# Optimization experiments

Measured on AMD Instinct MI355X. Metric: run time of the kernel, lower is better.

## Reference

```python
import jax, jax.numpy as jnp
import numpy as np

DIM = 768
NH = 12
HD = DIM // NH
MLP = 4 * DIM
EPS = 1e-5


def _ln(x, w, b):
    mu = x.mean(-1, keepdims=True)
    var = ((x - mu) ** 2).mean(-1, keepdims=True)
    return (x - mu) * jax.lax.rsqrt(var + EPS) * w + b


def setup_inputs() -> dict:
    key = jax.random.key(0)
    ks = jax.random.split(key, 12)
    s = 0.02
    return {
        "xq": jax.random.normal(ks[0], (4, 32, 32, DIM), jnp.float32),
        "xkv": jax.random.normal(ks[1], (4, 64, 64, DIM), jnp.float32),
        "norm1_w": jnp.ones((DIM,), jnp.float32),
        "norm1_b": jnp.zeros((DIM,), jnp.float32),
        "kv_w": jax.random.normal(ks[2], (DIM, 2 * DIM), jnp.float32) * s,
        "kv_b": jnp.zeros((2 * DIM,), jnp.float32),
        "q_w": jax.random.normal(ks[3], (DIM, DIM), jnp.float32) * s,
        "q_b": jnp.zeros((DIM,), jnp.float32),
        "proj_w": jax.random.normal(ks[4], (DIM, DIM), jnp.float32) * s,
        "proj_b": jnp.zeros((DIM,), jnp.float32),
        "norm2_w": jnp.ones((DIM,), jnp.float32),
        "norm2_b": jnp.zeros((DIM,), jnp.float32),
        "mlp_w1": jax.random.normal(ks[5], (DIM, MLP), jnp.float32) * s,
        "mlp_b1": jnp.zeros((MLP,), jnp.float32),
        "mlp_w2": jax.random.normal(ks[6], (MLP, DIM), jnp.float32) * s,
        "mlp_b2": jnp.zeros((DIM,), jnp.float32),
    }


def reference(xq, xkv, norm1_w, norm1_b, kv_w, kv_b, q_w, q_b, proj_w, proj_b,
              norm2_w, norm2_b, mlp_w1, mlp_b1, mlp_w2, mlp_b2):
    B, Hq, Wq, C = xq.shape
    _, H, W, _ = xkv.shape
    shortcut = xq
    xn = _ln(xq, norm1_w, norm1_b)
    # kv projection: [B, H*W, 2, NH, HD]
    kv = (xkv.reshape(B, H * W, C) @ kv_w + kv_b).reshape(B, H * W, 2, NH, HD)
    k = kv[:, :, 0].transpose(0, 2, 1, 3)  # [B, NH, HW, HD]
    v = kv[:, :, 1].transpose(0, 2, 1, 3)
    q = (xn.reshape(B, Hq * Wq, C) @ q_w + q_b).reshape(B, Hq * Wq, NH, HD).transpose(0, 2, 1, 3)
    scale = HD ** -0.5
    attn = jnp.einsum('bhqd,bhkd->bhqk', q * scale, k)
    attn = jax.nn.softmax(attn, axis=-1)
    o = jnp.einsum('bhqk,bhkd->bhqd', attn, v)  # [B, NH, HqWq, HD]
    o = o.transpose(0, 2, 1, 3).reshape(B, Hq, Wq, C)
    o = o @ proj_w + proj_b
    x = shortcut + o
    xn2 = _ln(x, norm2_w, norm2_b)
    mlp = jax.nn.gelu(xn2 @ mlp_w1 + mlp_b1, approximate=False) @ mlp_w2 + mlp_b2
    return x + mlp
```

## Files before the change

kernel.cpp:

```cpp
#include <hip/hip_runtime.h>
#include <hip/hip_bf16.h>
#include <math.h>

#define DIM 768
#define NH 12
#define HD 64
#define NQ 1024
#define NKV 4096
#define QSCALE 0.18033688011112042f

typedef __attribute__((ext_vector_type(4))) float f32x4;
typedef __attribute__((ext_vector_type(16))) float f32x16;
typedef __attribute__((ext_vector_type(8))) __bf16 bf16x8;
typedef __attribute__((ext_vector_type(8))) unsigned short u16x8;
typedef __attribute__((ext_vector_type(4))) unsigned short u16x4;
typedef unsigned short u16;

typedef const __attribute__((address_space(1))) void* gas_t;
typedef __attribute__((address_space(3))) void* las_t;

__device__ __forceinline__ void gl16(const void* g, void* l) {
    __builtin_amdgcn_global_load_lds((gas_t)g, (las_t)l, 16, 0, 0);
}

__device__ __forceinline__ u16 f2b(float x) {
    __bf16 h = (__bf16)x;
    return __builtin_bit_cast(u16, h);
}

__device__ __forceinline__ float b2f(u16 x) {
    unsigned int u = ((unsigned int)x) << 16;
    return __builtin_bit_cast(float, u);
}

__device__ __forceinline__ f32x4 mfma16(const u16* a, const u16* b, f32x4 c) {
    bf16x8 av = *reinterpret_cast<const bf16x8*>(a);
    bf16x8 bv = *reinterpret_cast<const bf16x8*>(b);
    return __builtin_amdgcn_mfma_f32_16x16x32_bf16(av, bv, c, 0, 0, 0);
}

__device__ __forceinline__ f32x16 mfma32(bf16x8 a, bf16x8 b, f32x16 c) {
    return __builtin_amdgcn_mfma_f32_32x32x16_bf16(a, b, c, 0, 0, 0);
}

__global__ __launch_bounds__(256) void prep_kernel(
    const float* __restrict__ xkv, u16* __restrict__ xkv_b,
    const float* __restrict__ kvw, u16* __restrict__ wkv_bf,
    const float* __restrict__ qw,  u16* __restrict__ wq_bf,
    const float* __restrict__ pjw, u16* __restrict__ wpj_bf,
    const float* __restrict__ w1,  u16* __restrict__ w1_bf,
    const float* __restrict__ w2,  u16* __restrict__ w2_bf,
    const float* __restrict__ xq,  const float* __restrict__ n1w,
    const float* __restrict__ n1b, u16* __restrict__ xn_bf)
{
    __shared__ u16 T[64][72];
    int b = blockIdx.x, tid = threadIdx.x;
    if (b < 6144) {
        int i = b * 256 + tid;
        const float4* p = reinterpret_cast<const float4*>(xkv) + (size_t)i * 2;
        float4 a = p[0], bb = p[1];
        u16x8 o;
        o[0] = f2b(a.x); o[1] = f2b(a.y); o[2] = f2b(a.z); o[3] = f2b(a.w);
        o[4] = f2b(bb.x); o[5] = f2b(bb.y); o[6] = f2b(bb.z); o[7] = f2b(bb.w);
        reinterpret_cast<u16x8*>(xkv_b)[i] = o;
        return;
    }
    if (b < 7872) {
        int b2 = b - 6144;
        const float* W; u16* Wt; int K, N, nbx, base;
        if (b2 < 288)       { W = kvw; Wt = wkv_bf; K = 768;  N = 1536; nbx = 24; base = 0; }
        else if (b2 < 432)  { W = qw;  Wt = wq_bf;  K = 768;  N = 768;  nbx = 12; base = 288; }
        else if (b2 < 576)  { W = pjw; Wt = wpj_bf; K = 768;  N = 768;  nbx = 12; base = 432; }
        else if (b2 < 1152) { W = w1;  Wt = w1_bf;  K = 768;  N = 3072; nbx = 48; base = 576; }
        else                { W = w2;  Wt = w2_bf;  K = 3072; N = 768;  nbx = 12; base = 1152; }
        int bb2 = b2 - base;
        int bx = bb2 % nbx, by = bb2 / nbx;
        int k0 = by * 64, n0 = bx * 64;
        int r = tid >> 2, c = (tid & 3) * 16;
        const float* src = W + (size_t)(k0 + r) * N + n0 + c;
        #pragma unroll
        for (int j = 0; j < 16; j += 4) {
            float4 f = *reinterpret_cast<const float4*>(src + j);
            T[r][c + j + 0] = f2b(f.x); T[r][c + j + 1] = f2b(f.y);
            T[r][c + j + 2] = f2b(f.z); T[r][c + j + 3] = f2b(f.w);
        }
        __syncthreads();
        int d = tid >> 2, c2 = (tid & 3) * 16;
        u16x8 o0, o1;
        #pragma unroll
        for (int j = 0; j < 8; ++j) o0[j] = T[c2 + j][d];
        #pragma unroll
        for (int j = 0; j < 8; ++j) o1[j] = T[c2 + 8 + j][d];
        u16* dst = Wt + (size_t)(n0 + d) * K + k0 + c2;
        *reinterpret_cast<u16x8*>(dst) = o0;
        *reinterpret_cast<u16x8*>(dst + 8) = o1;
        return;
    }
    int row = b - 7872;
    const float* xr = xq + (size_t)row * DIM;
    float v0 = xr[tid], v1 = xr[tid + 256], v2 = xr[tid + 512];
    float s = v0 + v1 + v2;
    float s2 = v0 * v0 + v1 * v1 + v2 * v2;
    for (int off = 1; off < 64; off <<= 1) {
        s += __shfl_xor(s, off);
        s2 += __shfl_xor(s2, off);
    }
    float* ss = reinterpret_cast<float*>(&T[0][0]);
    float* ss2 = ss + 4;
    int wid = tid >> 6, lane = tid & 63;
    if (lane == 0) { ss[wid] = s; ss2[wid] = s2; }
    __syncthreads();
    s = ss[0] + ss[1] + ss[2] + ss[3];
    s2 = ss2[0] + ss2[1] + ss2[2] + ss2[3];
    float mu = s * (1.0f / DIM);
    float var = s2 * (1.0f / DIM) - mu * mu;
    float r = rsqrtf(var + 1e-5f);
    u16* orow = xn_bf + (size_t)row * DIM;
    orow[tid]       = f2b((v0 - mu) * r * n1w[tid]       + n1b[tid]);
    orow[tid + 256] = f2b((v1 - mu) * r * n1w[tid + 256] + n1b[tid + 256]);
    orow[tid + 512] = f2b((v2 - mu) * r * n1w[tid + 512] + n1b[tid + 512]);
}

__global__ __launch_bounds__(256) void ln_kernel(
    const float* __restrict__ x, const float* __restrict__ w,
    const float* __restrict__ b, u16* __restrict__ out)
{
    int row = blockIdx.x;
    const float* xr = x + (size_t)row * DIM;
    int tid = threadIdx.x;
    float v0 = xr[tid], v1 = xr[tid + 256], v2 = xr[tid + 512];
    float s = v0 + v1 + v2;
    float s2 = v0 * v0 + v1 * v1 + v2 * v2;
    for (int off = 1; off < 64; off <<= 1) {
        s += __shfl_xor(s, off);
        s2 += __shfl_xor(s2, off);
    }
    __shared__ float ss[4], ss2[4];
    int wid = tid >> 6, lane = tid & 63;
    if (lane == 0) { ss[wid] = s; ss2[wid] = s2; }
    __syncthreads();
    s = ss[0] + ss[1] + ss[2] + ss[3];
    s2 = ss2[0] + ss2[1] + ss2[2] + ss2[3];
    float mu = s * (1.0f / DIM);
    float var = s2 * (1.0f / DIM) - mu * mu;
    float r = rsqrtf(var + 1e-5f);
    u16* orow = out + (size_t)row * DIM;
    orow[tid]       = f2b((v0 - mu) * r * w[tid]       + b[tid]);
    orow[tid + 256] = f2b((v1 - mu) * r * w[tid + 256] + b[tid + 256]);
    orow[tid + 512] = f2b((v2 - mu) * r * w[tid + 512] + b[tid + 512]);
}

template <int EPI>
__global__ __launch_bounds__(256) void gemm_kernel(
    const u16* __restrict__ A, const u16* __restrict__ Bt,
    const float* __restrict__ bias, const float* __restrict__ res,
    void* __restrict__ out, void* __restrict__ out2, int M, int N, int K)
{
    __shared__ u16 As[3][4096];
    __shared__ u16 Bs[3][4096];
    int p = blockIdx.x;
    int nbx = N >> 7;
    int ypx = (M >> 7) >> 3;
    int xcd = p & 7, slot = p >> 3;
    int by = xcd * ypx + slot / nbx;
    int bx = slot - (slot / nbx) * nbx;
    int n0 = bx * 128, m0 = by * 128;
    int tid = threadIdx.x, lane = tid & 63, wave = tid >> 6;
    int wm = (wave >> 1) * 64, wn = (wave & 1) * 64;
    f32x4 acc[4][4] = {};

    int ca = tid, cb = tid + 256;
    int ra = ca >> 2, sa = ((ca & 3) ^ (ra & 3)) * 8;
    int rb = cb >> 2, sb = ((cb & 3) ^ (rb & 3)) * 8;
    const u16* Asrc1 = A + (size_t)(m0 + ra) * K + sa;
    const u16* Asrc2 = A + (size_t)(m0 + rb) * K + sb;
    const u16* Bsrc1 = Bt + (size_t)(n0 + ra) * K + sa;
    const u16* Bsrc2 = Bt + (size_t)(n0 + rb) * K + sb;

    auto STAGE = [&](int buf, int k0) {
        gl16(Asrc1 + k0, &As[buf][ca * 8]);
        gl16(Asrc2 + k0, &As[buf][cb * 8]);
        gl16(Bsrc1 + k0, &Bs[buf][ca * 8]);
        gl16(Bsrc2 + k0, &Bs[buf][cb * 8]);
    };

    int fr = lane & 15, fq = lane >> 4;
    int co = (fq ^ (fr & 3)) * 8;

    auto COMPUTE = [&](int buf) {
        #pragma unroll
        for (int mf = 0; mf < 4; ++mf) {
            const u16* a = &As[buf][(wm + mf * 16 + fr) * 32 + co];
            #pragma unroll
            for (int nf = 0; nf < 4; ++nf)
                acc[mf][nf] = mfma16(a, &Bs[buf][(wn + nf * 16 + fr) * 32 + co],
                                     acc[mf][nf]);
        }
    };

    int NIT = K >> 5;
    STAGE(0, 0);
    STAGE(1, 32);
    asm volatile("s_waitcnt vmcnt(4)" ::: "memory");
    __builtin_amdgcn_s_barrier();
    int cur = 0;
    for (int it = 0; it < NIT; ++it) {
        int pre = (cur >= 1) ? cur - 1 : 2;
        bool more = (it + 2 < NIT);
        if (more) STAGE(pre, (it + 2) << 5);
        COMPUTE(cur);
        if (more) { asm volatile("s_waitcnt vmcnt(4)" ::: "memory"); }
        else      { asm volatile("s_waitcnt vmcnt(0)" ::: "memory"); }
        __builtin_amdgcn_s_barrier();
        cur = (cur == 2) ? 0 : cur + 1;
    }

    if constexpr (EPI == 4) {
        u16* kb = reinterpret_cast<u16*>(out);
        u16* vtb = reinterpret_cast<u16*>(out2);
        if (n0 < 768) {
            #pragma unroll
            for (int mf = 0; mf < 4; ++mf)
                #pragma unroll
                for (int nf = 0; nf < 4; ++nf) {
                    int col = n0 + wn + nf * 16 + fr;
                    float bv = bias[col];
                    #pragma unroll
                    for (int r = 0; r < 4; ++r) {
                        int row = m0 + wm + mf * 16 + fq * 4 + r;
                        kb[(size_t)row * 768 + col] = f2b(acc[mf][nf][r] + bv);
                    }
                }
        } else {
            #pragma unroll
            for (int mf = 0; mf < 4; ++mf)
                #pragma unroll
                for (int nf = 0; nf < 4; ++nf) {
                    int col = n0 + wn + nf * 16 + fr;
                    int c = col - 768, h = c >> 6, d = c & 63;
                    float bv = bias[col];
                    int row0 = m0 + wm + mf * 16 + fq * 4;
                    int bb = row0 >> 12, kvi = row0 & 4095;
                    int kv6 = kvi & 63;
                    int slot = (kv6 & 51) | ((kv6 & 4) << 1) | ((kv6 & 8) >> 1);
                    u16x4 pv;
                    #pragma unroll
                    for (int r = 0; r < 4; ++r) pv[r] = f2b(acc[mf][nf][r] + bv);
                    *reinterpret_cast<u16x4*>(vtb + ((size_t)(bb * 12 + h) * 64 + d) * 4096
                                              + (kvi & ~63) + slot) = pv;
                }
        }
        return;
    }

    float* outf = reinterpret_cast<float*>(out);
    u16* outb = reinterpret_cast<u16*>(out);
    #pragma unroll
    for (int mf = 0; mf < 4; ++mf)
        #pragma unroll
        for (int nf = 0; nf < 4; ++nf)
            #pragma unroll
            for (int r = 0; r < 4; ++r) {
                int row = m0 + wm + mf * 16 + fq * 4 + r;
                int col = n0 + wn + nf * 16 + fr;
                size_t idx = (size_t)row * N + col;
                float v = acc[mf][nf][r] + bias[col];
                if constexpr (EPI == 2) {
                    outf[idx] = v + res[idx];
                } else {
                    float g = v / (1.0f + __expf(-1.702f * v));
                    outb[idx] = f2b(g);
                }
            }
}

template <int EPI>
__global__ __launch_bounds__(256) void gemm64_kernel(
    const u16* __restrict__ A, const u16* __restrict__ Bt,
    const float* __restrict__ bias, const float* __restrict__ res,
    void* __restrict__ out, int M, int N, int K)
{
    __shared__ u16 As[3][4096];
    __shared__ u16 Bs[3][4096];
    int p = blockIdx.x;
    int nbx = N >> 6;
    int ypx = (M >> 6) >> 3;
    int xcd = p & 7, slot = p >> 3;
    int by = xcd * ypx + slot / nbx;
    int bx = slot - (slot / nbx) * nbx;
    int n0 = bx * 64, m0 = by * 64;
    int tid = threadIdx.x, lane = tid & 63, wave = tid >> 6;
    int wm = (wave >> 1) * 32, wn = (wave & 1) * 32;
    f32x4 acc[2][2] = {};

    int c1 = tid, c2 = tid + 256;
    int r1 = c1 >> 3, s1 = ((c1 & 7) ^ (r1 & 7)) * 8;
    int r2 = c2 >> 3, s2 = ((c2 & 7) ^ (r2 & 7)) * 8;
    const u16* As1 = A + (size_t)(m0 + r1) * K + s1;
    const u16* As2 = A + (size_t)(m0 + r2) * K + s2;
    const u16* Bt1 = Bt + (size_t)(n0 + r1) * K + s1;
    const u16* Bt2 = Bt + (size_t)(n0 + r2) * K + s2;

    auto STAGE = [&](int buf, int k0) {
        gl16(As1 + k0, &As[buf][c1 * 8]);
        gl16(As2 + k0, &As[buf][c2 * 8]);
        gl16(Bt1 + k0, &Bs[buf][c1 * 8]);
        gl16(Bt2 + k0, &Bs[buf][c2 * 8]);
    };

    int fr = lane & 15, fq = lane >> 4;
    int co0 = (fq ^ (fr & 7)) * 8;
    int co1 = ((4 + fq) ^ (fr & 7)) * 8;

    int NIT = K >> 6;
    STAGE(0, 0);
    STAGE(1, 64);
    asm volatile("s_waitcnt vmcnt(4)" ::: "memory");
    __builtin_amdgcn_s_barrier();
    int cur = 0;
    for (int it = 0; it < NIT; ++it) {
        int pre = (cur >= 1) ? cur - 1 : 2;
        bool more = (it + 2 < NIT);
        if (more) STAGE(pre, (it + 2) << 6);
        #pragma unroll
        for (int mf = 0; mf < 2; ++mf) {
            const u16* arow = &As[cur][(wm + mf * 16 + fr) * 64];
            #pragma unroll
            for (int nf = 0; nf < 2; ++nf) {
                const u16* brow = &Bs[cur][(wn + nf * 16 + fr) * 64];
                acc[mf][nf] = mfma16(arow + co0, brow + co0, acc[mf][nf]);
                acc[mf][nf] = mfma16(arow + co1, brow + co1, acc[mf][nf]);
            }
        }
        if (more) { asm volatile("s_waitcnt vmcnt(4)" ::: "memory"); }
        else      { asm volatile("s_waitcnt vmcnt(0)" ::: "memory"); }
        __builtin_amdgcn_s_barrier();
        cur = (cur == 2) ? 0 : cur + 1;
    }

    float* outf = reinterpret_cast<float*>(out);
    u16* outb = reinterpret_cast<u16*>(out);
    #pragma unroll
    for (int mf = 0; mf < 2; ++mf)
        #pragma unroll
        for (int nf = 0; nf < 2; ++nf)
            #pragma unroll
            for (int r = 0; r < 4; ++r) {
                int row = m0 + wm + mf * 16 + fq * 4 + r;
                int col = n0 + wn + nf * 16 + fr;
                size_t idx = (size_t)row * N + col;
                float v = acc[mf][nf][r] + bias[col];
                if constexpr (EPI == 1) {
                    outb[idx] = f2b(v * QSCALE);
                } else {
                    outf[idx] = v + res[idx];
                }
            }
}

__global__ __launch_bounds__(256, 4) void attn_kernel(
    const u16* __restrict__ q, const u16* __restrict__ kbuf,
    const u16* __restrict__ vt, u16* __restrict__ op0, u16* __restrict__ op1,
    u16* __restrict__ op2, u16* __restrict__ op3, float* __restrict__ L)
{
    int p = blockIdx.x;
    int xcd = p & 7, slot = p >> 3;
    int bh = xcd * 6 + (slot >> 5);
    int rem = slot & 31;
    int qt = rem >> 2, quarter = rem & 3;
    int h = bh % NH, bb = bh / NH;
    const int NIT = 16;

    __shared__ u16 Kb[2][4096];
    __shared__ u16 Vb[2][4096];

    int tid = threadIdx.x, lane = tid & 63, wave = tid >> 6;
    int l31 = lane & 31, hi = lane >> 5;
    int sw = l31 & 7;

    u16x8 ov = {0x3F80, 0x3F80, 0x3F80, 0x3F80, 0x3F80, 0x3F80, 0x3F80, 0x3F80};
    const bf16x8 ONES = __builtin_bit_cast(bf16x8, ov);

    bf16x8 qf[4];
    {
        const u16* qbp = q + (size_t)(bb * NQ + qt * 128 + wave * 32 + l31) * DIM
                         + h * HD + hi * 8;
        #pragma unroll
        for (int ks = 0; ks < 4; ++ks)
            qf[ks] = *reinterpret_cast<const bf16x8*>(qbp + ks * 16);
    }

    int c1 = tid, c2 = tid + 256;
    int r1 = c1 >> 3, sc1 = (c1 & 7) ^ (r1 & 7);
    int r2 = c2 >> 3, sc2 = (c2 & 7) ^ (r2 & 7);
    size_t krow0 = (size_t)bb * NKV + quarter * 1024;
    const u16* ks1 = kbuf + (krow0 + r1) * 768 + h * HD + sc1 * 8;
    const u16* ks2 = kbuf + (krow0 + r2) * 768 + h * HD + sc2 * 8;
    const u16* vs1 = vt + ((size_t)bh * HD + r1) * NKV + quarter * 1024 + sc1 * 8;
    const u16* vs2 = vt + ((size_t)bh * HD + r2) * NKV + quarter * 1024 + sc2 * 8;

    auto STAGE = [&](int buf, int kv0) {
        gl16(ks1 + (size_t)kv0 * 768, &Kb[buf][c1 * 8]);
        gl16(ks2 + (size_t)kv0 * 768, &Kb[buf][c2 * 8]);
        gl16(vs1 + kv0, &Vb[buf][c1 * 8]);
        gl16(vs2 + kv0, &Vb[buf][c2 * 8]);
    };

    f32x16 oacc0 = {}, oacc1 = {}, lsum = {};

    STAGE(0, 0);
    asm volatile("s_waitcnt vmcnt(0)" ::: "memory");
    __builtin_amdgcn_s_barrier();

    auto BODY = [&](int cur, int it) {
        if (it + 1 < NIT) STAGE(cur ^ 1, (it + 1) * 64);
        const u16* vb = &Vb[cur][l31 * 64];
        #pragma unroll
        for (int kh = 0; kh < 2; ++kh) {
            const u16* kb = &Kb[cur][(kh * 32 + l31) * 64];
            f32x16 s = {};
            __builtin_amdgcn_s_setprio(1);
            #pragma unroll
            for (int ks = 0; ks < 4; ++ks) {
                bf16x8 kf = *reinterpret_cast<const bf16x8*>(
                    kb + (((ks * 2 + hi) ^ sw) * 8));
                s = mfma32(kf, qf[ks], s);
            }
            __builtin_amdgcn_s_setprio(0);
            u16x8 p0, p1;
            #pragma unroll
            for (int r = 0; r < 8; ++r) p0[r] = f2b(exp2f(s[r]));
            #pragma unroll
            for (int r = 0; r < 8; ++r) p1[r] = f2b(exp2f(s[r + 8]));
            bf16x8 a0 = __builtin_bit_cast(bf16x8, p0);
            bf16x8 a1 = __builtin_bit_cast(bf16x8, p1);
            int vc0 = ((kh * 4 + 0 + hi) ^ sw) * 8;
            int vc1 = ((kh * 4 + 2 + hi) ^ sw) * 8;
            __builtin_amdgcn_s_setprio(1);
            lsum = mfma32(a0, ONES, lsum);
            lsum = mfma32(a1, ONES, lsum);
            bf16x8 v00 = *reinterpret_cast<const bf16x8*>(vb + vc0);
            bf16x8 v01 = *reinterpret_cast<const bf16x8*>(vb + vc1);
            bf16x8 v10 = *reinterpret_cast<const bf16x8*>(vb + 2048 + vc0);
            bf16x8 v11 = *reinterpret_cast<const bf16x8*>(vb + 2048 + vc1);
            oacc0 = mfma32(a0, v00, oacc0);
            oacc0 = mfma32(a1, v01, oacc0);
            oacc1 = mfma32(a0, v10, oacc1);
            oacc1 = mfma32(a1, v11, oacc1);
            __builtin_amdgcn_s_setprio(0);
        }
        asm volatile("s_waitcnt vmcnt(0)" ::: "memory");
        __builtin_amdgcn_s_barrier();
    };

    for (int it = 0; it < NIT; it += 2) { BODY(0, it); BODY(1, it + 1); }

    u16* op = (quarter == 0) ? op0 : (quarter == 1) ? op1 : (quarter == 2) ? op2 : op3;
    #pragma unroll
    for (int r = 0; r < 16; ++r) {
        int qrow = (r & 3) + 8 * (r >> 2) + 4 * hi;
        float rcl = 1.0f / lsum[r];
        size_t orow = (size_t)(bb * NQ + qt * 128 + wave * 32 + qrow) * DIM + h * HD;
        op[orow + l31] = f2b(oacc0[r] * rcl);
        op[orow + 32 + l31] = f2b(oacc1[r] * rcl);
    }
    if (l31 == 0) {
        #pragma unroll
        for (int r = 0; r < 16; ++r) {
            int qrow = (r & 3) + 8 * (r >> 2) + 4 * hi;
            L[quarter * 49152 + bh * 1024 + qt * 128 + wave * 32 + qrow] = lsum[r];
        }
    }
}

__global__ __launch_bounds__(256) void combine_kernel(
    const u16* __restrict__ op0, const u16* __restrict__ op1,
    const u16* __restrict__ op2, const u16* __restrict__ op3,
    const float* __restrict__ L, u16* __restrict__ out)
{
    int idx = blockIdx.x * 256 + threadIdx.x;
    int t = idx / 96, cc = (idx - t * 96) * 8;
    int h = cc >> 6;
    int bb = t >> 10, qr = t & 1023;
    int li = (bb * 12 + h) * 1024 + qr;
    float l0 = L[li], l1 = L[49152 + li], l2 = L[2 * 49152 + li], l3 = L[3 * 49152 + li];
    float rs = 1.0f / (l0 + l1 + l2 + l3);
    u16x8 a = *reinterpret_cast<const u16x8*>(op0 + (size_t)t * 768 + cc);
    u16x8 b = *reinterpret_cast<const u16x8*>(op1 + (size_t)t * 768 + cc);
    u16x8 c = *reinterpret_cast<const u16x8*>(op2 + (size_t)t * 768 + cc);
    u16x8 d = *reinterpret_cast<const u16x8*>(op3 + (size_t)t * 768 + cc);
    u16x8 o;
    #pragma unroll
    for (int j = 0; j < 8; ++j)
        o[j] = f2b((b2f(a[j]) * l0 + b2f(b[j]) * l1 + b2f(c[j]) * l2 + b2f(d[j]) * l3) * rs);
    *reinterpret_cast<u16x8*>(out + (size_t)t * 768 + cc) = o;
}

extern "C" void kernel_launch(void* const* d_in, const int* in_sizes, int n_in,
                              void* d_out, int out_size, void* d_ws, size_t ws_size,
                              hipStream_t stream) {
    const float* xq  = (const float*)d_in[0];
    const float* xkv = (const float*)d_in[1];
    const float* n1w = (const float*)d_in[2];
    const float* n1b = (const float*)d_in[3];
    const float* kvw = (const float*)d_in[4];
    const float* kvb = (const float*)d_in[5];
    const float* qw  = (const float*)d_in[6];
    const float* qb  = (const float*)d_in[7];
    const float* pjw = (const float*)d_in[8];
    const float* pjb = (const float*)d_in[9];
    const float* n2w = (const float*)d_in[10];
    const float* n2b = (const float*)d_in[11];
    const float* w1  = (const float*)d_in[12];
    const float* b1  = (const float*)d_in[13];
    const float* w2  = (const float*)d_in[14];
    const float* b2  = (const float*)d_in[15];
    float* xout = (float*)d_out;

    char* ws = (char*)d_ws;
    u16* xkv_b  = (u16*)(ws);
    u16* kbuf   = (u16*)(ws + 25165824);
    u16* vt     = (u16*)(ws + 50331648);
    u16* xn_bf  = (u16*)(ws + 75497472);
    u16* q_bf   = (u16*)(ws + 81788928);
    u16* o_bf   = (u16*)(ws + 88080384);
    u16* wkv_bf = (u16*)(ws + 94371840);
    u16* wq_bf  = (u16*)(ws + 96731136);
    u16* wpj_bf = (u16*)(ws + 97910784);
    u16* w1_bf  = (u16*)(ws + 99090432);
    u16* w2_bf  = (u16*)(ws + 103809024);
    u16* hid    = xkv_b;
    u16* op2    = xkv_b;
    u16* op3    = (u16*)(ws + 6291456);
    float* Lbuf = (float*)wkv_bf;

    prep_kernel<<<dim3(11968), dim3(256), 0, stream>>>(
        xkv, xkv_b, kvw, wkv_bf, qw, wq_bf, pjw, wpj_bf, w1, w1_bf, w2, w2_bf,
        xq, n1w, n1b, xn_bf);
    gemm_kernel<4><<<dim3(12 * 128), dim3(256), 0, stream>>>(xkv_b, wkv_bf, kvb, nullptr, kbuf, vt, 16384, 1536, 768);
    gemm64_kernel<1><<<dim3(768), dim3(256), 0, stream>>>(xn_bf, wq_bf, qb, nullptr, q_bf, 4096, 768, 768);
    attn_kernel<<<dim3(1536), dim3(256), 0, stream>>>(q_bf, kbuf, vt, xn_bf, o_bf, op2, op3, Lbuf);
    combine_kernel<<<dim3(1536), dim3(256), 0, stream>>>(xn_bf, o_bf, op2, op3, Lbuf, q_bf);
    gemm64_kernel<2><<<dim3(768), dim3(256), 0, stream>>>(q_bf, wpj_bf, pjb, xq, xout, 4096, 768, 768);
    ln_kernel<<<dim3(4096), dim3(256), 0, stream>>>(xout, n2w, n2b, xn_bf);
    gemm_kernel<3><<<dim3(24 * 32), dim3(256), 0, stream>>>(xn_bf, w1_bf, b1, nullptr, hid, nullptr, 4096, 3072, 768);
    gemm64_kernel<2><<<dim3(768), dim3(256), 0, stream>>>(hid, w2_bf, b2, xout, xout, 4096, 768, 3072);
}
```

Measured before the change: 271.2 us.

## Merge KV and Q projection GEMMs into one launch; split-K final MLP GEMM

The KV projection and the Q projection GEMMs now run in a single kernel launch, with blocks below 1536 doing the KV tile path and the remaining 768 doing the 64x64 Q path. This removes one launch and lets the smaller Q GEMM fill the tail of the KV GEMM. The final MLP down-projection is split along K into two halves across 1536 blocks, and each half accumulates into xout with float atomicAdd, relying on xout already holding the residual. This doubles the parallelism of the K=3072 GEMM, at the cost of atomic traffic and a summation order that is no longer deterministic.

```diff
diff --git a/kernel.cpp b/kernel.cpp
--- a/kernel.cpp
+++ b/kernel.cpp
@@ -150,11 +150,175 @@
     orow[tid + 512] = f2b((v2 - mu) * r * w[tid + 512] + b[tid + 512]);
 }
 
+__global__ __launch_bounds__(256) void qkv_gemm_kernel(
+    const u16* __restrict__ Akv, const u16* __restrict__ Wkv, const float* __restrict__ bkv,
+    u16* __restrict__ kbuf, u16* __restrict__ vtb,
+    const u16* __restrict__ Aq, const u16* __restrict__ Wq, const float* __restrict__ bq,
+    u16* __restrict__ qout)
+{
+    __shared__ u16 As[3][4096];
+    __shared__ u16 Bs[3][4096];
+    int tid = threadIdx.x, lane = tid & 63, wave = tid >> 6;
+    int fr = lane & 15, fq = lane >> 4;
+
+    if (blockIdx.x < 1536) {
+        const int K = 768;
+        int p = blockIdx.x;
+        int nbx = 12, ypx = 16;
+        int xcd = p & 7, slot = p >> 3;
+        int by = xcd * ypx + slot / nbx;
+        int bx = slot - (slot / nbx) * nbx;
+        int n0 = bx * 128, m0 = by * 128;
+        int wm = (wave >> 1) * 64, wn = (wave & 1) * 64;
+        f32x4 acc[4][4] = {};
+
+        int ca = tid, cb = tid + 256;
+        int ra = ca >> 2, sa = ((ca & 3) ^ (ra & 3)) * 8;
+        int rb = cb >> 2, sb = ((cb & 3) ^ (rb & 3)) * 8;
+        const u16* Asrc1 = Akv + (size_t)(m0 + ra) * K + sa;
+        const u16* Asrc2 = Akv + (size_t)(m0 + rb) * K + sb;
+        const u16* Bsrc1 = Wkv + (size_t)(n0 + ra) * K + sa;
+        const u16* Bsrc2 = Wkv + (size_t)(n0 + rb) * K + sb;
+
+        auto STAGE = [&](int buf, int k0) {
+            gl16(Asrc1 + k0, &As[buf][ca * 8]);
+            gl16(Asrc2 + k0, &As[buf][cb * 8]);
+            gl16(Bsrc1 + k0, &Bs[buf][ca * 8]);
+            gl16(Bsrc2 + k0, &Bs[buf][cb * 8]);
+        };
+        int co = (fq ^ (fr & 3)) * 8;
+
+        int NIT = K >> 5;
+        STAGE(0, 0);
+        STAGE(1, 32);
+        asm volatile("s_waitcnt vmcnt(4)" ::: "memory");
+        __builtin_amdgcn_s_barrier();
+        int cur = 0;
+        for (int it = 0; it < NIT; ++it) {
+            int pre = (cur >= 1) ? cur - 1 : 2;
+            bool more = (it + 2 < NIT);
+            if (more) STAGE(pre, (it + 2) << 5);
+            #pragma unroll
+            for (int mf = 0; mf < 4; ++mf) {
+                const u16* a = &As[cur][(wm + mf * 16 + fr) * 32 + co];
+                #pragma unroll
+                for (int nf = 0; nf < 4; ++nf)
+                    acc[mf][nf] = mfma16(a, &Bs[cur][(wn + nf * 16 + fr) * 32 + co],
+                                         acc[mf][nf]);
+            }
+            if (more) { asm volatile("s_waitcnt vmcnt(4)" ::: "memory"); }
+            else      { asm volatile("s_waitcnt vmcnt(0)" ::: "memory"); }
+            __builtin_amdgcn_s_barrier();
+            cur = (cur == 2) ? 0 : cur + 1;
+        }
+
+        if (n0 < 768) {
+            #pragma unroll
+            for (int mf = 0; mf < 4; ++mf)
+                #pragma unroll
+                for (int nf = 0; nf < 4; ++nf) {
+                    int col = n0 + wn + nf * 16 + fr;
+                    float bv = bkv[col];
+                    #pragma unroll
+                    for (int r = 0; r < 4; ++r) {
+                        int row = m0 + wm + mf * 16 + fq * 4 + r;
+                        kbuf[(size_t)row * 768 + col] = f2b(acc[mf][nf][r] + bv);
+                    }
+                }
+        } else {
+            #pragma unroll
+            for (int mf = 0; mf < 4; ++mf)
+                #pragma unroll
+                for (int nf = 0; nf < 4; ++nf) {
+                    int col = n0 + wn + nf * 16 + fr;
+                    int c = col - 768, h = c >> 6, d = c & 63;
+                    float bv = bkv[col];
+                    int row0 = m0 + wm + mf * 16 + fq * 4;
+                    int bb = row0 >> 12, kvi = row0 & 4095;
+                    int kv6 = kvi & 63;
+                    int slot2 = (kv6 & 51) | ((kv6 & 4) << 1) | ((kv6 & 8) >> 1);
+                    u16x4 pv;
+                    #pragma unroll
+                    for (int r = 0; r < 4; ++r) pv[r] = f2b(acc[mf][nf][r] + bv);
+                    *reinterpret_cast<u16x4*>(vtb + ((size_t)(bb * 12 + h) * 64 + d) * 4096
+                                              + (kvi & ~63) + slot2) = pv;
+                }
+        }
+        return;
+    }
+
+    {
+        const int K = 768;
+        int p = blockIdx.x - 1536;
+        int nbx = 12, ypx = 8;
+        int xcd = p & 7, slot = p >> 3;
+        int by = xcd * ypx + slot / nbx;
+        int bx = slot - (slot / nbx) * nbx;
+        int n0 = bx * 64, m0 = by * 64;
+        int wm = (wave >> 1) * 32, wn = (wave & 1) * 32;
+        f32x4 acc[2][2] = {};
+
+        int c1 = tid, c2 = tid + 256;
+        int r1 = c1 >> 3, s1 = ((c1 & 7) ^ (r1 & 7)) * 8;
+        int r2 = c2 >> 3, s2 = ((c2 & 7) ^ (r2 & 7)) * 8;
+        const u16* As1 = Aq + (size_t)(m0 + r1) * K + s1;
+        const u16* As2 = Aq + (size_t)(m0 + r2) * K + s2;
+        const u16* Bt1 = Wq + (size_t)(n0 + r1) * K + s1;
+        const u16* Bt2 = Wq + (size_t)(n0 + r2) * K + s2;
+
+        auto STAGE = [&](int buf, int k0) {
+            gl16(As1 + k0, &As[buf][c1 * 8]);
+            gl16(As2 + k0, &As[buf][c2 * 8]);
+            gl16(Bt1 + k0, &Bs[buf][c1 * 8]);
+            gl16(Bt2 + k0, &Bs[buf][c2 * 8]);
+        };
+        int co0 = (fq ^ (fr & 7)) * 8;
+        int co1 = ((4 + fq) ^ (fr & 7)) * 8;
+
+        int NIT = K >> 6;
+        STAGE(0, 0);
+        STAGE(1, 64);
+        asm volatile("s_waitcnt vmcnt(4)" ::: "memory");
+        __builtin_amdgcn_s_barrier();
+        int cur = 0;
+        for (int it = 0; it < NIT; ++it) {
+            int pre = (cur >= 1) ? cur - 1 : 2;
+            bool more = (it + 2 < NIT);
+            if (more) STAGE(pre, (it + 2) << 6);
+            #pragma unroll
+            for (int mf = 0; mf < 2; ++mf) {
+                const u16* arow = &As[cur][(wm + mf * 16 + fr) * 64];
+                #pragma unroll
+                for (int nf = 0; nf < 2; ++nf) {
+                    const u16* brow = &Bs[cur][(wn + nf * 16 + fr) * 64];
+                    acc[mf][nf] = mfma16(arow + co0, brow + co0, acc[mf][nf]);
+                    acc[mf][nf] = mfma16(arow + co1, brow + co1, acc[mf][nf]);
+                }
+            }
+            if (more) { asm volatile("s_waitcnt vmcnt(4)" ::: "memory"); }
+            else      { asm volatile("s_waitcnt vmcnt(0)" ::: "memory"); }
+            __builtin_amdgcn_s_barrier();
+            cur = (cur == 2) ? 0 : cur + 1;
+        }
+
+        #pragma unroll
+        for (int mf = 0; mf < 2; ++mf)
+            #pragma unroll
+            for (int nf = 0; nf < 2; ++nf)
+                #pragma unroll
+                for (int r = 0; r < 4; ++r) {
+                    int row = m0 + wm + mf * 16 + fq * 4 + r;
+                    int col = n0 + wn + nf * 16 + fr;
+                    qout[(size_t)row * 768 + col] = f2b((acc[mf][nf][r] + bq[col]) * QSCALE);
+                }
+    }
+}
+
 template <int EPI>
 __global__ __launch_bounds__(256) void gemm_kernel(
     const u16* __restrict__ A, const u16* __restrict__ Bt,
     const float* __restrict__ bias, const float* __restrict__ res,
-    void* __restrict__ out, void* __restrict__ out2, int M, int N, int K)
+    void* __restrict__ out, int M, int N, int K)
 {
     __shared__ u16 As[3][4096];
     __shared__ u16 Bs[3][4096];
@@ -187,17 +351,6 @@
     int fr = lane & 15, fq = lane >> 4;
     int co = (fq ^ (fr & 3)) * 8;
 
-    auto COMPUTE = [&](int buf) {
-        #pragma unroll
-        for (int mf = 0; mf < 4; ++mf) {
-            const u16* a = &As[buf][(wm + mf * 16 + fr) * 32 + co];
-            #pragma unroll
-            for (int nf = 0; nf < 4; ++nf)
-                acc[mf][nf] = mfma16(a, &Bs[buf][(wn + nf * 16 + fr) * 32 + co],
-                                     acc[mf][nf]);
-        }
-    };
-
     int NIT = K >> 5;
     STAGE(0, 0);
     STAGE(1, 32);
@@ -208,49 +361,18 @@
         int pre = (cur >= 1) ? cur - 1 : 2;
         bool more = (it + 2 < NIT);
         if (more) STAGE(pre, (it + 2) << 5);
-        COMPUTE(cur);
+        #pragma unroll
+        for (int mf = 0; mf < 4; ++mf) {
+            const u16* a = &As[cur][(wm + mf * 16 + fr) * 32 + co];
+            #pragma unroll
+            for (int nf = 0; nf < 4; ++nf)
+                acc[mf][nf] = mfma16(a, &Bs[cur][(wn + nf * 16 + fr) * 32 + co],
+                                     acc[mf][nf]);
+        }
         if (more) { asm volatile("s_waitcnt vmcnt(4)" ::: "memory"); }
         else      { asm volatile("s_waitcnt vmcnt(0)" ::: "memory"); }
         __builtin_amdgcn_s_barrier();
         cur = (cur == 2) ? 0 : cur + 1;
-    }
-
-    if constexpr (EPI == 4) {
-        u16* kb = reinterpret_cast<u16*>(out);
-        u16* vtb = reinterpret_cast<u16*>(out2);
-        if (n0 < 768) {
-            #pragma unroll
-            for (int mf = 0; mf < 4; ++mf)
-                #pragma unroll
-                for (int nf = 0; nf < 4; ++nf) {
-                    int col = n0 + wn + nf * 16 + fr;
-                    float bv = bias[col];
-                    #pragma unroll
-                    for (int r = 0; r < 4; ++r) {
-                        int row = m0 + wm + mf * 16 + fq * 4 + r;
-                        kb[(size_t)row * 768 + col] = f2b(acc[mf][nf][r] + bv);
-                    }
-                }
-        } else {
-            #pragma unroll
-            for (int mf = 0; mf < 4; ++mf)
-                #pragma unroll
-                for (int nf = 0; nf < 4; ++nf) {
-                    int col = n0 + wn + nf * 16 + fr;
-                    int c = col - 768, h = c >> 6, d = c & 63;
-                    float bv = bias[col];
-                    int row0 = m0 + wm + mf * 16 + fq * 4;
-                    int bb = row0 >> 12, kvi = row0 & 4095;
-                    int kv6 = kvi & 63;
-                    int slot = (kv6 & 51) | ((kv6 & 4) << 1) | ((kv6 & 8) >> 1);
-                    u16x4 pv;
-                    #pragma unroll
-                    for (int r = 0; r < 4; ++r) pv[r] = f2b(acc[mf][nf][r] + bv);
-                    *reinterpret_cast<u16x4*>(vtb + ((size_t)(bb * 12 + h) * 64 + d) * 4096
-                                              + (kvi & ~63) + slot) = pv;
-                }
-        }
-        return;
     }
 
     float* outf = reinterpret_cast<float*>(out);
@@ -274,11 +396,10 @@
             }
 }
 
-template <int EPI>
 __global__ __launch_bounds__(256) void gemm64_kernel(
     const u16* __restrict__ A, const u16* __restrict__ Bt,
     const float* __restrict__ bias, const float* __restrict__ res,
-    void* __restrict__ out, int M, int N, int K)
+    float* __restrict__ out, int M, int N, int K)
 {
     __shared__ u16 As[3][4096];
     __shared__ u16 Bs[3][4096];
@@ -338,8 +459,6 @@
         cur = (cur == 2) ? 0 : cur + 1;
     }
 
-    float* outf = reinterpret_cast<float*>(out);
-    u16* outb = reinterpret_cast<u16*>(out);
     #pragma unroll
     for (int mf = 0; mf < 2; ++mf)
         #pragma unroll
@@ -349,12 +468,86 @@
                 int row = m0 + wm + mf * 16 + fq * 4 + r;
                 int col = n0 + wn + nf * 16 + fr;
                 size_t idx = (size_t)row * N + col;
-                float v = acc[mf][nf][r] + bias[col];
-                if constexpr (EPI == 1) {
-                    outb[idx] = f2b(v * QSCALE);
-                } else {
-                    outf[idx] = v + res[idx];
-                }
+                out[idx] = acc[mf][nf][r] + bias[col] + res[idx];
+            }
+}
+
+__global__ __launch_bounds__(256) void mlp2_kernel(
+    const u16* __restrict__ A, const u16* __restrict__ Bt,
+    const float* __restrict__ bias, float* __restrict__ out, int M, int N, int K)
+{
+    __shared__ u16 As[3][4096];
+    __shared__ u16 Bs[3][4096];
+    int pb = blockIdx.x;
+    int kh = pb >= 768;
+    int p = pb - (kh ? 768 : 0);
+    int kOff = kh ? (K >> 1) : 0;
+    int KH = K >> 1;
+    int nbx = N >> 6;
+    int ypx = (M >> 6) >> 3;
+    int xcd = p & 7, slot = p >> 3;
+    int by = xcd * ypx + slot / nbx;
+    int bx = slot - (slot / nbx) * nbx;
+    int n0 = bx * 64, m0 = by * 64;
+    int tid = threadIdx.x, lane = tid & 63, wave = tid >> 6;
+    int wm = (wave >> 1) * 32, wn = (wave & 1) * 32;
+    f32x4 acc[2][2] = {};
+
+    int c1 = tid, c2 = tid + 256;
+    int r1 = c1 >> 3, s1 = ((c1 & 7) ^ (r1 & 7)) * 8;
+    int r2 = c2 >> 3, s2 = ((c2 & 7) ^ (r2 & 7)) * 8;
+    const u16* As1 = A + (size_t)(m0 + r1) * K + kOff + s1;
+    const u16* As2 = A + (size_t)(m0 + r2) * K + kOff + s2;
+    const u16* Bt1 = Bt + (size_t)(n0 + r1) * K + kOff + s1;
+    const u16* Bt2 = Bt + (size_t)(n0 + r2) * K + kOff + s2;
+
+    auto STAGE = [&](int buf, int k0) {
+        gl16(As1 + k0, &As[buf][c1 * 8]);
+        gl16(As2 + k0, &As[buf][c2 * 8]);
+        gl16(Bt1 + k0, &Bs[buf][c1 * 8]);
+        gl16(Bt2 + k0, &Bs[buf][c2 * 8]);
+    };
+
+    int fr = lane & 15, fq = lane >> 4;
+    int co0 = (fq ^ (fr & 7)) * 8;
+    int co1 = ((4 + fq) ^ (fr & 7)) * 8;
+
+    int NIT = KH >> 6;
+    STAGE(0, 0);
+    STAGE(1, 64);
+    asm volatile("s_waitcnt vmcnt(4)" ::: "memory");
+    __builtin_amdgcn_s_barrier();
+    int cur = 0;
+    for (int it = 0; it < NIT; ++it) {
+        int pre = (cur >= 1) ? cur - 1 : 2;
+        bool more = (it + 2 < NIT);
+        if (more) STAGE(pre, (it + 2) << 6);
+        #pragma unroll
+        for (int mf = 0; mf < 2; ++mf) {
+            const u16* arow = &As[cur][(wm + mf * 16 + fr) * 64];
+            #pragma unroll
+            for (int nf = 0; nf < 2; ++nf) {
+                const u16* brow = &Bs[cur][(wn + nf * 16 + fr) * 64];
+                acc[mf][nf] = mfma16(arow + co0, brow + co0, acc[mf][nf]);
+                acc[mf][nf] = mfma16(arow + co1, brow + co1, acc[mf][nf]);
+            }
+        }
+        if (more) { asm volatile("s_waitcnt vmcnt(4)" ::: "memory"); }
+        else      { asm volatile("s_waitcnt vmcnt(0)" ::: "memory"); }
+        __builtin_amdgcn_s_barrier();
+        cur = (cur == 2) ? 0 : cur + 1;
+    }
+
+    #pragma unroll
+    for (int mf = 0; mf < 2; ++mf)
+        #pragma unroll
+        for (int nf = 0; nf < 2; ++nf)
+            #pragma unroll
+            for (int r = 0; r < 4; ++r) {
+                int row = m0 + wm + mf * 16 + fq * 4 + r;
+                int col = n0 + wn + nf * 16 + fr;
+                float v = acc[mf][nf][r] + (kh ? 0.0f : bias[col]);
+                atomicAdd(out + (size_t)row * N + col, v);
             }
 }
 
@@ -537,12 +730,12 @@
     prep_kernel<<<dim3(11968), dim3(256), 0, stream>>>(
         xkv, xkv_b, kvw, wkv_bf, qw, wq_bf, pjw, wpj_bf, w1, w1_bf, w2, w2_bf,
         xq, n1w, n1b, xn_bf);
-    gemm_kernel<4><<<dim3(12 * 128), dim3(256), 0, stream>>>(xkv_b, wkv_bf, kvb, nullptr, kbuf, vt, 16384, 1536, 768);
-    gemm64_kernel<1><<<dim3(768), dim3(256), 0, stream>>>(xn_bf, wq_bf, qb, nullptr, q_bf, 4096, 768, 768);
+    qkv_gemm_kernel<<<dim3(2304), dim3(256), 0, stream>>>(
+        xkv_b, wkv_bf, kvb, kbuf, vt, xn_bf, wq_bf, qb, q_bf);
     attn_kernel<<<dim3(1536), dim3(256), 0, stream>>>(q_bf, kbuf, vt, xn_bf, o_bf, op2, op3, Lbuf);
     combine_kernel<<<dim3(1536), dim3(256), 0, stream>>>(xn_bf, o_bf, op2, op3, Lbuf, q_bf);
-    gemm64_kernel<2><<<dim3(768), dim3(256), 0, stream>>>(q_bf, wpj_bf, pjb, xq, xout, 4096, 768, 768);
+    gemm64_kernel<<<dim3(768), dim3(256), 0, stream>>>(q_bf, wpj_bf, pjb, xq, xout, 4096, 768, 768);
     ln_kernel<<<dim3(4096), dim3(256), 0, stream>>>(xout, n2w, n2b, xn_bf);
-    gemm_kernel<3><<<dim3(24 * 32), dim3(256), 0, stream>>>(xn_bf, w1_bf, b1, nullptr, hid, nullptr, 4096, 3072, 768);
-    gemm64_kernel<2><<<dim3(768), dim3(256), 0, stream>>>(hid, w2_bf, b2, xout, xout, 4096, 768, 3072);
-}
+    gemm_kernel<3><<<dim3(24 * 32), dim3(256), 0, stream>>>(xn_bf, w1_bf, b1, nullptr, hid, 4096, 3072, 768);
+    mlp2_kernel<<<dim3(1536), dim3(256), 0, stream>>>(hid, w2_bf, b2, xout, 4096, 768, 3072);
+}
```

Result: slower. 292.1 us (+7.7%).
